# Kernel optimization log

Hardware: AMD Instinct MI355X
Metric: run time of the kernel (lower is better)

The kernel has to match this reference:

```python
import jax, jax.numpy as jnp
import numpy as np

N_NODES = 50000
N_EDGES = 1600000
IN_DIM = 128
N_HEADS = 8
OUT_DIM = 16
LEAKY_SLOPE = 0.2


def setup_inputs() -> dict:
    key = jax.random.key(0)
    k1, k2, k3, k4, k5, k6 = jax.random.split(key, 6)
    x = jax.random.normal(k1, (N_NODES, IN_DIM), dtype=jnp.float32)
    W = jax.random.normal(k2, (N_HEADS * OUT_DIM, IN_DIM), dtype=jnp.float32) * (1.414 / np.sqrt(IN_DIM))
    attn_l = jax.random.normal(k3, (N_HEADS, OUT_DIM), dtype=jnp.float32) * 0.5
    attn_r = jax.random.normal(k4, (N_HEADS, OUT_DIM), dtype=jnp.float32) * 0.5
    src = jax.random.randint(k5, (N_EDGES,), 0, N_NODES, dtype=jnp.int64) if jax.config.jax_enable_x64 else jax.random.randint(k5, (N_EDGES,), 0, N_NODES, dtype=jnp.int32)
    dst = jax.random.randint(k6, (N_EDGES,), 0, N_NODES, dtype=src.dtype)
    return {"x": x, "W": W, "attn_l": attn_l, "attn_r": attn_r, "src": src, "dst": dst}


def reference(x, W, attn_l, attn_r, src, dst):
    n = x.shape[0]
    # fc projection -> [N, H, D]
    ft = (x @ W.T).reshape(n, N_HEADS, OUT_DIM)
    # per-node attention logits (bmm with [H,D,1] vector == contraction over D) -> [N, H]
    a1 = jnp.einsum('nhd,hd->nh', ft, attn_l)
    a2 = jnp.einsum('nhd,hd->nh', ft, attn_r)
    # per-edge score: leaky_relu(a1[src] + a2[dst]) -> [E, H]
    e = jax.nn.leaky_relu(a1[src] + a2[dst], negative_slope=LEAKY_SLOPE)
    # segment softmax over incoming edges of each dst node (numerically stable)
    seg_max = jax.ops.segment_max(e, dst, num_segments=n)          # [N, H]
    seg_max = jnp.where(jnp.isfinite(seg_max), seg_max, 0.0)       # isolated nodes -> 0
    e_exp = jnp.exp(e - seg_max[dst])                              # [E, H]
    denom = jax.ops.segment_sum(e_exp, dst, num_segments=n)        # [N, H]
    alpha = e_exp / denom[dst]                                     # [E, H]
    # weighted scatter-sum of src messages -> [N, H, D]
    msgs = ft[src] * alpha[:, :, None]                             # [E, H, D]
    out = jax.ops.segment_sum(msgs, dst, num_segments=n)
    return out
```

## Files before the change

### kernel.cpp

```cpp
#include <hip/hip_runtime.h>
#include <math.h>

#define N_NODES 50000
#define N_EDGES 1600000
#define IN_DIM 128
#define N_HEADS 8
#define OUT_DIM 16
#define HD 128
#define NBUCK 784
#define BCAP 2560
#define CHUNK 4096
#define BIN_BLOCKS ((N_EDGES + CHUNK - 1) / CHUNK)
#define NTILE 3125
#define PBLK ((NTILE + 3) / 4)
#define TROW 132
#define LOG2E 1.4426950408889634f
#define NPH 7
#define AGG_BLOCKS 1024
#define AGG_WAVES (AGG_BLOCKS * 4)
#define NPW 13

typedef __attribute__((ext_vector_type(8))) short bf16x8;
typedef __attribute__((ext_vector_type(4))) float f32x4;

__device__ __forceinline__ unsigned short f2bf(float f) {
    union { float f; unsigned int u; } v; v.f = f;
    unsigned int u = v.u;
    unsigned int r = (u + 0x7fffu + ((u >> 16) & 1u)) >> 16;
    return (unsigned short)r;
}

__device__ __forceinline__ void scan_nbuck_excl(int* arr, int* part) {
    int t = threadIdx.x;
    int v0 = 0, v1 = 0, v2 = 0, v3 = 0, cs = 0;
    if (t < NBUCK / 4) {
        v0 = arr[4 * t]; v1 = arr[4 * t + 1]; v2 = arr[4 * t + 2]; v3 = arr[4 * t + 3];
        cs = v0 + v1 + v2 + v3;
    }
    part[t] = cs;
    __syncthreads();
    for (int d = 1; d < 256; d <<= 1) {
        int u = (t >= d) ? part[t - d] : 0;
        __syncthreads();
        part[t] += u;
        __syncthreads();
    }
    if (t < NBUCK / 4) {
        int run = part[t] - cs;
        arr[4 * t] = run; run += v0;
        arr[4 * t + 1] = run; run += v1;
        arr[4 * t + 2] = run; run += v2;
        arr[4 * t + 3] = run;
    }
    __syncthreads();
}

__global__ void k_prep(const float* __restrict__ W, unsigned short* __restrict__ Wb,
                       int* __restrict__ bucket_cnt, int* __restrict__ ovf_cnt,
                       unsigned short* __restrict__ ftb, float* __restrict__ a1) {
    int g = blockIdx.x * 256 + threadIdx.x;
    if (g < NBUCK) bucket_cnt[g] = 0;
    if (g == 0) *ovf_cnt = 0;
    if (g < 64) ((unsigned int*)(ftb + (size_t)N_NODES * HD))[g] = 0u;
    if (g >= 64 && g < 64 + N_HEADS)
        a1[(size_t)N_NODES * N_HEADS + (g - 64)] = __int_as_float(0xff800000);
    if (g >= (HD * IN_DIM) / 4) return;
    float4 v = ((const float4*)W)[g];
    ushort4 us;
    us.x = f2bf(v.x); us.y = f2bf(v.y); us.z = f2bf(v.z); us.w = f2bf(v.w);
    ((ushort4*)Wb)[g] = us;
}

__global__ __launch_bounds__(256) void k_proj_bin(
    const float* __restrict__ x, const unsigned short* __restrict__ Wb,
    const float* __restrict__ attn_l, const float* __restrict__ attn_r,
    unsigned short* __restrict__ ftb, float* __restrict__ a1, float* __restrict__ a2,
    const int* __restrict__ src, const int* __restrict__ dst,
    unsigned int* __restrict__ region, int* __restrict__ bucket_cnt,
    int* __restrict__ ovf_cnt, unsigned int* __restrict__ ovf) {
    __shared__ __align__(16) char smem[4 * 16 * TROW * 4];
    int tid = threadIdx.x;

    if (blockIdx.x < PBLK) {
        int wid  = tid >> 6;
        int tile = blockIdx.x * 4 + wid;
        if (tile >= NTILE) return;
        int lane = tid & 63;
        int m = lane & 15, q = lane >> 4;
        int node0 = tile * 16;

        const float* xr = x + (size_t)(node0 + m) * IN_DIM + q * 8;
        float4 xa[4][2];
#pragma unroll
        for (int ks = 0; ks < 4; ks++) {
            xa[ks][0] = *(const float4*)(xr + ks * 32);
            xa[ks][1] = *(const float4*)(xr + ks * 32 + 4);
        }
        bf16x8 afr[4];
#pragma unroll
        for (int ks = 0; ks < 4; ks++) {
            afr[ks][0] = (short)f2bf(xa[ks][0].x); afr[ks][1] = (short)f2bf(xa[ks][0].y);
            afr[ks][2] = (short)f2bf(xa[ks][0].z); afr[ks][3] = (short)f2bf(xa[ks][0].w);
            afr[ks][4] = (short)f2bf(xa[ks][1].x); afr[ks][5] = (short)f2bf(xa[ks][1].y);
            afr[ks][6] = (short)f2bf(xa[ks][1].z); afr[ks][7] = (short)f2bf(xa[ks][1].w);
        }

        float* tl = (float*)smem + wid * (16 * TROW);

#pragma unroll
        for (int h = 0; h < N_HEADS; h++) {
            const unsigned short* wrow = Wb + (size_t)(h * 16 + m) * IN_DIM + q * 8;
            f32x4 c = {0.f, 0.f, 0.f, 0.f};
#pragma unroll
            for (int ks = 0; ks < 4; ks++) {
                bf16x8 bfr = *(const bf16x8*)(wrow + ks * 32);
                c = __builtin_amdgcn_mfma_f32_16x16x32_bf16(afr[ks], bfr, c, 0, 0, 0);
            }
#pragma unroll
            for (int r = 0; r < 4; r++)
                tl[(q * 4 + r) * TROW + h * 16 + m] = c[r];
        }

        int nd = lane & 15;
#pragma unroll
        for (int hi = 0; hi < 2; hi++) {
            int hh = (lane >> 4) + hi * 4;
            const float4* rowv = (const float4*)(tl + nd * TROW + hh * 16);
            const float4* alv  = (const float4*)(attn_l + hh * OUT_DIM);
            const float4* arv  = (const float4*)(attn_r + hh * OUT_DIM);
            float sl = 0.f, sr = 0.f;
#pragma unroll
            for (int d4 = 0; d4 < 4; d4++) {
                float4 fv = rowv[d4];
                float4 al = alv[d4];
                float4 ar = arv[d4];
                sl += fv.x * al.x + fv.y * al.y + fv.z * al.z + fv.w * al.w;
                sr += fv.x * ar.x + fv.y * ar.y + fv.z * ar.z + fv.w * ar.w;
            }
            a1[(node0 + nd) * N_HEADS + hh] = sl * LOG2E;
            a2[(node0 + nd) * N_HEADS + hh] = sr * LOG2E;
        }

#pragma unroll
        for (int p = 0; p < 4; p++) {
            int r = p * 4 + q;
            const float* srcp = tl + r * TROW + m * 8;
            float4 f0 = *(const float4*)(srcp);
            float4 f1 = *(const float4*)(srcp + 4);
            ushort4 u0, u1;
            u0.x = f2bf(f0.x); u0.y = f2bf(f0.y); u0.z = f2bf(f0.z); u0.w = f2bf(f0.w);
            u1.x = f2bf(f1.x); u1.y = f2bf(f1.y); u1.z = f2bf(f1.z); u1.w = f2bf(f1.w);
            ushort4* dstp = (ushort4*)(ftb + (size_t)(node0 + r) * HD + m * 8);
            dstp[0] = u0;
            dstp[1] = u1;
        }
    } else {
        unsigned int* stage = (unsigned int*)smem;
        int* hist  = (int*)(smem + 16384);
        int* delta = (int*)(smem + 19520);
        int* part  = (int*)(smem + 22656);

        int t = tid;
        int base = (blockIdx.x - PBLK) * CHUNK;
        int nvalid = min(CHUNK, N_EDGES - base);

        for (int i = t; i < NBUCK; i += 256) hist[i] = 0;
        __syncthreads();

        unsigned int mypack[CHUNK / 256];
#pragma unroll
        for (int k = 0; k < CHUNK / 256; k++) {
            int i = t + k * 256;
            if (i < nvalid) {
                int s = src[base + i];
                int d = dst[base + i];
                unsigned int p = ((unsigned int)d << 16) | (unsigned int)s;
                mypack[k] = p;
                atomicAdd(&hist[d >> 6], 1);
            }
        }
        __syncthreads();
        for (int i = t; i < NBUCK; i += 256) {
            int h = hist[i];
            delta[i] = (h > 0) ? atomicAdd(&bucket_cnt[i], h) : 0;
        }
        __syncthreads();
        scan_nbuck_excl(hist, part);
        for (int i = t; i < NBUCK; i += 256) delta[i] -= hist[i];
        __syncthreads();
#pragma unroll
        for (int k = 0; k < CHUNK / 256; k++) {
            int i = t + k * 256;
            if (i < nvalid) {
                unsigned int p = mypack[k];
                int slot = atomicAdd(&hist[p >> 22], 1);
                stage[slot] = p;
            }
        }
        __syncthreads();
        for (int i = t; i < nvalid; i += 256) {
            unsigned int p = stage[i];
            int b = p >> 22;
            int pos = delta[b] + i;
            if (pos < BCAP) region[(size_t)b * BCAP + pos] = p;
            else { int o = atomicAdd(ovf_cnt, 1); ovf[o] = p; }
        }
    }
}

__global__ __launch_bounds__(256) void k_place(
    const unsigned int* __restrict__ region, const int* __restrict__ bucket_cnt,
    const int* __restrict__ ovf_cnt, const unsigned int* __restrict__ ovf,
    int* __restrict__ nps, unsigned short* __restrict__ esrc) {
    int b = blockIdx.x;
    int t = threadIdx.x;
    __shared__ int sb[NBUCK], part[256];
    __shared__ int hist[512], sc[512], curs[64 * NPH];
    __shared__ unsigned short sstage[BCAP];

    for (int i = t; i < NBUCK; i += 256) sb[i] = bucket_cnt[i];
    for (int i = t; i < 512; i += 256) hist[i] = 0;
    __syncthreads();
    scan_nbuck_excl(sb, part);

    int truec = bucket_cnt[b];
    int base_b = sb[b];
    int rc = min(truec, BCAP);
    bool fits = (truec <= BCAP);
    const unsigned int* reg = region + (size_t)b * BCAP;

    for (int i = t; i < rc; i += 256) {
        unsigned int p = reg[i];
        int key = (int)((p >> 16) & 63) * NPH + (int)((p & 0xffffu) >> 13);
        atomicAdd(&hist[key], 1);
    }
    int no = 0;
    if (truec > BCAP) {
        no = *ovf_cnt;
        for (int i = t; i < no; i += 256)
            if ((int)(ovf[i] >> 22) == b) {
                unsigned int p = ovf[i];
                int key = (int)((p >> 16) & 63) * NPH + (int)((p & 0xffffu) >> 13);
                atomicAdd(&hist[key], 1);
            }
    }
    __syncthreads();

    {
        int h0 = hist[2 * t], h1 = hist[2 * t + 1];
        int ps = h0 + h1;
        part[t] = ps;
        __syncthreads();
        for (int d = 1; d < 256; d <<= 1) {
            int u = (t >= d) ? part[t - d] : 0;
            __syncthreads();
            part[t] += u;
            __syncthreads();
        }
        int run = part[t] - ps;
        sc[2 * t] = run;
        sc[2 * t + 1] = run + h0;
    }
    __syncthreads();

    for (int i = t; i < 64 * NPH; i += 256) curs[i] = base_b + sc[i];
    for (int i = t; i < 512; i += 256) {
        int nl = i >> 3, p = i & 7;
        int node = b * 64 + nl;
        if (node < N_NODES) {
            int v = (p < NPH) ? sc[nl * NPH + p] : sc[(nl + 1) * NPH];
            nps[node * 8 + p] = base_b + v;
        }
    }
    __syncthreads();

    for (int i = t; i < rc; i += 256) {
        unsigned int p = reg[i];
        int key = (int)((p >> 16) & 63) * NPH + (int)((p & 0xffffu) >> 13);
        int pos = atomicAdd(&curs[key], 1);
        if (fits) sstage[pos - base_b] = (unsigned short)(p & 0xffffu);
        else      esrc[pos] = (unsigned short)(p & 0xffffu);
    }
    if (truec > BCAP) {
        for (int i = t; i < no; i += 256) {
            unsigned int p = ovf[i];
            if ((int)(p >> 22) == b) {
                int key = (int)((p >> 16) & 63) * NPH + (int)((p & 0xffffu) >> 13);
                int pos = atomicAdd(&curs[key], 1);
                esrc[pos] = (unsigned short)(p & 0xffffu);
            }
        }
    }
    __syncthreads();
    if (fits) {
        for (int i = t; i < truec; i += 256)
            esrc[base_b + i] = sstage[i];
    }
}

__global__ __launch_bounds__(256, 4) void k_aggregate(
    const unsigned short* __restrict__ ftb, const float* __restrict__ a1,
    const float* __restrict__ a2, const int* __restrict__ nps,
    const unsigned short* __restrict__ esrc, float* __restrict__ out) {
    int wid  = threadIdx.x >> 6;
    int lane = threadIdx.x & 63;
    int gw = blockIdx.x * 4 + wid;
    int hl = lane >> 3;
    int dimoff = lane * 2;

    int node_l = gw + lane * AGG_WAVES;
    bool vld = (lane < NPW) && (node_l < N_NODES);

    float accx[NPW], accy[NPW], l[NPW], a2h[NPW];
#pragma unroll
    for (int i = 0; i < NPW; i++) {
        accx[i] = 0.f; accy[i] = 0.f; l[i] = 0.f;
        int node = gw + i * AGG_WAVES;
        a2h[i] = (node < N_NODES) ? a2[node * N_HEADS + hl] : 0.f;
    }

    for (int p = 0; p < NPH; p++) {
        int stv = vld ? nps[node_l * 8 + p] : 0;
        int env = vld ? nps[node_l * 8 + p + 1] : 0;
#pragma unroll
        for (int i = 0; i < NPW; i++) {
            int st = __builtin_amdgcn_readlane(stv, i);
            int en = __builtin_amdgcn_readlane(env, i);
            for (int base = st; base < en; base += 64) {
                int nbc = en - base; if (nbc > 64) nbc = 64;
                int v = (int)esrc[base + lane];
                int sv = (lane < nbc) ? v : N_NODES;
                for (int done = 0; done < nbc; done += 8) {
                    float a1v[8]; unsigned int pv[8];
#pragma unroll
                    for (int k = 0; k < 8; k++) {
                        int s = __builtin_amdgcn_readlane(sv, done + k);
                        a1v[k] = a1[(size_t)s * N_HEADS + hl];
                        pv[k]  = *(const unsigned int*)(ftb + (size_t)s * HD + dimoff);
                    }
#pragma unroll
                    for (int k = 0; k < 8; k++) {
                        float tt = a1v[k] + a2h[i];
                        float u = fmaxf(tt, 0.2f * tt);
                        float e;
                        asm("v_exp_f32 %0, %1" : "=v"(e) : "v"(u));
                        l[i] += e;
                        accx[i] = fmaf(e, __uint_as_float(pv[k] << 16), accx[i]);
                        accy[i] = fmaf(e, __uint_as_float(pv[k] & 0xffff0000u), accy[i]);
                    }
                }
            }
        }
    }

    int d0v = vld ? nps[node_l * 8 + 0] : 0;
    int d7v = vld ? nps[node_l * 8 + 7] : 0;
#pragma unroll
    for (int i = 0; i < NPW; i++) {
        int node = gw + i * AGG_WAVES;
        if (node >= N_NODES) break;
        int deg = __builtin_amdgcn_readlane(d7v, i) - __builtin_amdgcn_readlane(d0v, i);
        float invl = (deg > 0) ? 1.f / l[i] : 0.f;
        float2 o; o.x = accx[i] * invl; o.y = accy[i] * invl;
        *(float2*)(out + (size_t)node * HD + dimoff) = o;
    }
}

extern "C" void kernel_launch(void* const* d_in, const int* in_sizes, int n_in,
                              void* d_out, int out_size, void* d_ws, size_t ws_size,
                              hipStream_t stream) {
    const float* x      = (const float*)d_in[0];
    const float* W      = (const float*)d_in[1];
    const float* attn_l = (const float*)d_in[2];
    const float* attn_r = (const float*)d_in[3];
    const int*   src    = (const int*)d_in[4];
    const int*   dst    = (const int*)d_in[5];
    float* out = (float*)d_out;

    char* ws = (char*)d_ws;
    size_t o = 0;
    auto alloc = [&](size_t bytes) -> char* {
        char* p = ws + o;
        o = (o + bytes + 255) & ~(size_t)255;
        return p;
    };
    unsigned short* ftb  = (unsigned short*)alloc((size_t)(N_NODES + 1) * HD * 2);
    float* a1            = (float*)alloc((size_t)(N_NODES + 1) * N_HEADS * 4);
    float* a2            = (float*)alloc((size_t)N_NODES * N_HEADS * 4);
    unsigned short* Wb   = (unsigned short*)alloc((size_t)HD * IN_DIM * 2);
    unsigned int* region = (unsigned int*)alloc((size_t)NBUCK * BCAP * 4);
    int* bucket_cnt      = (int*)alloc((size_t)NBUCK * 4);
    int* ovf_cnt         = (int*)alloc(4);
    unsigned int* ovf    = (unsigned int*)alloc((size_t)N_EDGES * 4);
    int* nps             = (int*)alloc((size_t)N_NODES * 8 * 4);
    unsigned short* esrc = (unsigned short*)alloc((size_t)N_EDGES * 2 + 256);

    (void)in_sizes; (void)n_in; (void)out_size; (void)ws_size;

    k_prep<<<16, 256, 0, stream>>>(W, Wb, bucket_cnt, ovf_cnt, ftb, a1);
    k_proj_bin<<<PBLK + BIN_BLOCKS, 256, 0, stream>>>(
        x, Wb, attn_l, attn_r, ftb, a1, a2,
        src, dst, region, bucket_cnt, ovf_cnt, ovf);
    k_place<<<NBUCK, 256, 0, stream>>>(region, bucket_cnt, ovf_cnt, ovf, nps, esrc);
    k_aggregate<<<AGG_BLOCKS, 256, 0, stream>>>(ftb, a1, a2, nps, esrc, out);
}
```

Baseline: 232.2 us.

## Reorder edge list phase-major globally and stream contiguous node ranges per wave

```diff
diff --git a/kernel.cpp b/kernel.cpp
--- a/kernel.cpp
+++ b/kernel.cpp
@@ -16,6 +16,7 @@
 #define TROW 132
 #define LOG2E 1.4426950408889634f
 #define NPH 7
+#define NB2 (NPH * NBUCK)
 #define AGG_BLOCKS 1024
 #define AGG_WAVES (AGG_BLOCKS * 4)
 #define NPW 13
@@ -55,11 +56,35 @@
     __syncthreads();
 }
 
+__device__ __forceinline__ void scan_flat_excl(int* arr, int n, int* part) {
+    int t = threadIdx.x;
+    int K = (n + 255) / 256;
+    int base = t * K;
+    int cs = 0;
+    for (int k = 0; k < K; k++) { int idx = base + k; if (idx < n) cs += arr[idx]; }
+    part[t] = cs;
+    __syncthreads();
+    for (int d = 1; d < 256; d <<= 1) {
+        int u = (t >= d) ? part[t - d] : 0;
+        __syncthreads();
+        part[t] += u;
+        __syncthreads();
+    }
+    int run = part[t] - cs;
+    for (int k = 0; k < K; k++) {
+        int idx = base + k;
+        if (idx < n) { int v = arr[idx]; arr[idx] = run; run += v; }
+    }
+    __syncthreads();
+}
+
 __global__ void k_prep(const float* __restrict__ W, unsigned short* __restrict__ Wb,
-                       int* __restrict__ bucket_cnt, int* __restrict__ ovf_cnt,
+                       int* __restrict__ bucket_cnt, int* __restrict__ cntp,
+                       int* __restrict__ ovf_cnt,
                        unsigned short* __restrict__ ftb, float* __restrict__ a1) {
     int g = blockIdx.x * 256 + threadIdx.x;
     if (g < NBUCK) bucket_cnt[g] = 0;
+    if (g < NB2) cntp[g] = 0;
     if (g == 0) *ovf_cnt = 0;
     if (g < 64) ((unsigned int*)(ftb + (size_t)N_NODES * HD))[g] = 0u;
     if (g >= 64 && g < 64 + N_HEADS)
@@ -77,7 +102,7 @@
     unsigned short* __restrict__ ftb, float* __restrict__ a1, float* __restrict__ a2,
     const int* __restrict__ src, const int* __restrict__ dst,
     unsigned int* __restrict__ region, int* __restrict__ bucket_cnt,
-    int* __restrict__ ovf_cnt, unsigned int* __restrict__ ovf) {
+    int* __restrict__ cntp, int* __restrict__ ovf_cnt, unsigned int* __restrict__ ovf) {
     __shared__ __align__(16) char smem[4 * 16 * TROW * 4];
     int tid = threadIdx.x;
 
@@ -177,6 +202,7 @@
                 unsigned int p = ((unsigned int)d << 16) | (unsigned int)s;
                 mypack[k] = p;
                 atomicAdd(&hist[d >> 6], 1);
+                atomicAdd(&cntp[(s >> 13) * NBUCK + (d >> 6)], 1);
             }
         }
         __syncthreads();
@@ -210,28 +236,30 @@
 
 __global__ __launch_bounds__(256) void k_place(
     const unsigned int* __restrict__ region, const int* __restrict__ bucket_cnt,
-    const int* __restrict__ ovf_cnt, const unsigned int* __restrict__ ovf,
-    int* __restrict__ nps, unsigned short* __restrict__ esrc) {
+    const int* __restrict__ cntp, const int* __restrict__ ovf_cnt,
+    const unsigned int* __restrict__ ovf,
+    int* __restrict__ nps2, unsigned short* __restrict__ esrc) {
     int b = blockIdx.x;
     int t = threadIdx.x;
-    __shared__ int sb[NBUCK], part[256];
-    __shared__ int hist[512], sc[512], curs[64 * NPH];
+    __shared__ int cpb[NB2], part[256];
+    __shared__ int hist[NPH * 64];
+    __shared__ int curs[NPH * 64];
+    __shared__ int gstart[NPH], lstart[NPH], phtot[NPH];
     __shared__ unsigned short sstage[BCAP];
 
-    for (int i = t; i < NBUCK; i += 256) sb[i] = bucket_cnt[i];
-    for (int i = t; i < 512; i += 256) hist[i] = 0;
-    __syncthreads();
-    scan_nbuck_excl(sb, part);
+    for (int i = t; i < NB2; i += 256) cpb[i] = cntp[i];
+    for (int i = t; i < NPH * 64; i += 256) hist[i] = 0;
+    __syncthreads();
+    scan_flat_excl(cpb, NB2, part);
 
     int truec = bucket_cnt[b];
-    int base_b = sb[b];
     int rc = min(truec, BCAP);
     bool fits = (truec <= BCAP);
     const unsigned int* reg = region + (size_t)b * BCAP;
 
     for (int i = t; i < rc; i += 256) {
-        unsigned int p = reg[i];
-        int key = (int)((p >> 16) & 63) * NPH + (int)((p & 0xffffu) >> 13);
+        unsigned int pk = reg[i];
+        int key = (int)((pk & 0xffffu) >> 13) * 64 + (int)((pk >> 16) & 63);
         atomicAdd(&hist[key], 1);
     }
     int no = 0;
@@ -239,68 +267,105 @@
         no = *ovf_cnt;
         for (int i = t; i < no; i += 256)
             if ((int)(ovf[i] >> 22) == b) {
-                unsigned int p = ovf[i];
-                int key = (int)((p >> 16) & 63) * NPH + (int)((p & 0xffffu) >> 13);
+                unsigned int pk = ovf[i];
+                int key = (int)((pk & 0xffffu) >> 13) * 64 + (int)((pk >> 16) & 63);
                 atomicAdd(&hist[key], 1);
             }
     }
     __syncthreads();
-
-    {
-        int h0 = hist[2 * t], h1 = hist[2 * t + 1];
-        int ps = h0 + h1;
-        part[t] = ps;
-        __syncthreads();
-        for (int d = 1; d < 256; d <<= 1) {
-            int u = (t >= d) ? part[t - d] : 0;
-            __syncthreads();
-            part[t] += u;
-            __syncthreads();
-        }
-        int run = part[t] - ps;
-        sc[2 * t] = run;
-        sc[2 * t + 1] = run + h0;
-    }
-    __syncthreads();
-
-    for (int i = t; i < 64 * NPH; i += 256) curs[i] = base_b + sc[i];
-    for (int i = t; i < 512; i += 256) {
-        int nl = i >> 3, p = i & 7;
+    scan_flat_excl(hist, NPH * 64, part);
+
+    if (t < NPH) {
+        gstart[t] = cpb[t * NBUCK + b];
+        lstart[t] = hist[t * 64];
+        phtot[t]  = ((t == NPH - 1) ? truec : hist[(t + 1) * 64]) - hist[t * 64];
+    }
+    __syncthreads();
+
+    for (int i = t; i < NPH * 64; i += 256) {
+        int p = i >> 6, nl = i & 63;
         int node = b * 64 + nl;
-        if (node < N_NODES) {
-            int v = (p < NPH) ? sc[nl * NPH + p] : sc[(nl + 1) * NPH];
-            nps[node * 8 + p] = base_b + v;
-        }
-    }
+        if (node < N_NODES)
+            nps2[(size_t)p * (N_NODES + 1) + node] = gstart[p] + (hist[i] - lstart[p]);
+        curs[i] = fits ? hist[i] : (gstart[p] + hist[i] - lstart[p]);
+    }
+    if (b == 0 && t < NPH)
+        nps2[(size_t)t * (N_NODES + 1) + N_NODES] =
+            (t == NPH - 1) ? N_EDGES : cpb[(t + 1) * NBUCK];
     __syncthreads();
 
     for (int i = t; i < rc; i += 256) {
-        unsigned int p = reg[i];
-        int key = (int)((p >> 16) & 63) * NPH + (int)((p & 0xffffu) >> 13);
+        unsigned int pk = reg[i];
+        int key = (int)((pk & 0xffffu) >> 13) * 64 + (int)((pk >> 16) & 63);
         int pos = atomicAdd(&curs[key], 1);
-        if (fits) sstage[pos - base_b] = (unsigned short)(p & 0xffffu);
-        else      esrc[pos] = (unsigned short)(p & 0xffffu);
+        if (fits) sstage[pos] = (unsigned short)(pk & 0xffffu);
+        else      esrc[pos]  = (unsigned short)(pk & 0xffffu);
     }
     if (truec > BCAP) {
         for (int i = t; i < no; i += 256) {
-            unsigned int p = ovf[i];
-            if ((int)(p >> 22) == b) {
-                int key = (int)((p >> 16) & 63) * NPH + (int)((p & 0xffffu) >> 13);
+            unsigned int pk = ovf[i];
+            if ((int)(pk >> 22) == b) {
+                int key = (int)((pk & 0xffffu) >> 13) * 64 + (int)((pk >> 16) & 63);
                 int pos = atomicAdd(&curs[key], 1);
-                esrc[pos] = (unsigned short)(p & 0xffffu);
+                esrc[pos] = (unsigned short)(pk & 0xffffu);
             }
         }
     }
     __syncthreads();
     if (fits) {
-        for (int i = t; i < truec; i += 256)
-            esrc[base_b + i] = sstage[i];
-    }
-}
+        for (int p = 0; p < NPH; p++)
+            for (int i = t; i < phtot[p]; i += 256)
+                esrc[gstart[p] + i] = sstage[lstart[p] + i];
+    }
+}
+
+template <int KK>
+__device__ __forceinline__ void issue8(int sv, const float* __restrict__ a1,
+                                       const unsigned short* __restrict__ ftb,
+                                       int hl, int dimoff,
+                                       float* a1v, unsigned int* pv) {
+#pragma unroll
+    for (int j = 0; j < 8; j++) {
+        int s = __builtin_amdgcn_readlane(sv, KK + j);
+        a1v[j] = a1[(size_t)s * N_HEADS + hl];
+        pv[j]  = *(const unsigned int*)(ftb + (size_t)s * HD + dimoff);
+    }
+}
+
+#define FLUSH_ADV()                                                         \
+    {                                                                       \
+        _Pragma("unroll")                                                   \
+        for (int q = 0; q < NPW; q++)                                       \
+            if (q == curi) {                                                \
+                accx[q] += tx; accy[q] += ty; lsum[q] += tl;                \
+                cura2 = (q + 1 < NPW) ? a2h[q + 1] : 0.f;                   \
+            }                                                               \
+        tx = ty = tl = 0.f;                                                 \
+    }
+
+#define CONSUME8(AV, PV, KK)                                                \
+    {                                                                       \
+        _Pragma("unroll")                                                   \
+        for (int j = 0; j < 8; j++) {                                       \
+            int pos = cb + (KK) + j;                                        \
+            while (curi < cnt - 1 && pos >= nb_end) {                       \
+                FLUSH_ADV();                                                \
+                curi++;                                                     \
+                nb_end = __builtin_amdgcn_readlane(bnd, curi + 1);          \
+            }                                                               \
+            float tt = AV[j] + cura2;                                       \
+            float uu = fmaxf(tt, 0.2f * tt);                                \
+            float ee;                                                       \
+            asm("v_exp_f32 %0, %1" : "=v"(ee) : "v"(uu));                   \
+            tl += ee;                                                       \
+            tx = fmaf(ee, __uint_as_float(PV[j] << 16), tx);                \
+            ty = fmaf(ee, __uint_as_float(PV[j] & 0xffff0000u), ty);        \
+        }                                                                   \
+    }
 
 __global__ __launch_bounds__(256, 4) void k_aggregate(
     const unsigned short* __restrict__ ftb, const float* __restrict__ a1,
-    const float* __restrict__ a2, const int* __restrict__ nps,
+    const float* __restrict__ a2, const int* __restrict__ nps2,
     const unsigned short* __restrict__ esrc, float* __restrict__ out) {
     int wid  = threadIdx.x >> 6;
     int lane = threadIdx.x & 63;
@@ -308,61 +373,68 @@
     int hl = lane >> 3;
     int dimoff = lane * 2;
 
-    int node_l = gw + lane * AGG_WAVES;
-    bool vld = (lane < NPW) && (node_l < N_NODES);
-
-    float accx[NPW], accy[NPW], l[NPW], a2h[NPW];
+    int n0 = __builtin_amdgcn_readfirstlane((int)(((long long)gw * N_NODES) / AGG_WAVES));
+    int n1 = __builtin_amdgcn_readfirstlane((int)(((long long)(gw + 1) * N_NODES) / AGG_WAVES));
+    int cnt = n1 - n0;
+
+    float accx[NPW], accy[NPW], lsum[NPW], a2h[NPW];
 #pragma unroll
     for (int i = 0; i < NPW; i++) {
-        accx[i] = 0.f; accy[i] = 0.f; l[i] = 0.f;
-        int node = gw + i * AGG_WAVES;
-        a2h[i] = (node < N_NODES) ? a2[node * N_HEADS + hl] : 0.f;
+        accx[i] = 0.f; accy[i] = 0.f; lsum[i] = 0.f;
+        int node = n0 + i; if (node > N_NODES - 1) node = N_NODES - 1;
+        a2h[i] = a2[(size_t)node * N_HEADS + hl];
     }
 
     for (int p = 0; p < NPH; p++) {
-        int stv = vld ? nps[node_l * 8 + p] : 0;
-        int env = vld ? nps[node_l * 8 + p + 1] : 0;
-#pragma unroll
-        for (int i = 0; i < NPW; i++) {
-            int st = __builtin_amdgcn_readlane(stv, i);
-            int en = __builtin_amdgcn_readlane(env, i);
-            for (int base = st; base < en; base += 64) {
-                int nbc = en - base; if (nbc > 64) nbc = 64;
-                int v = (int)esrc[base + lane];
-                int sv = (lane < nbc) ? v : N_NODES;
-                for (int done = 0; done < nbc; done += 8) {
-                    float a1v[8]; unsigned int pv[8];
-#pragma unroll
-                    for (int k = 0; k < 8; k++) {
-                        int s = __builtin_amdgcn_readlane(sv, done + k);
-                        a1v[k] = a1[(size_t)s * N_HEADS + hl];
-                        pv[k]  = *(const unsigned int*)(ftb + (size_t)s * HD + dimoff);
-                    }
-#pragma unroll
-                    for (int k = 0; k < 8; k++) {
-                        float tt = a1v[k] + a2h[i];
-                        float u = fmaxf(tt, 0.2f * tt);
-                        float e;
-                        asm("v_exp_f32 %0, %1" : "=v"(e) : "v"(u));
-                        l[i] += e;
-                        accx[i] = fmaf(e, __uint_as_float(pv[k] << 16), accx[i]);
-                        accy[i] = fmaf(e, __uint_as_float(pv[k] & 0xffff0000u), accy[i]);
-                    }
-                }
-            }
-        }
-    }
-
-    int d0v = vld ? nps[node_l * 8 + 0] : 0;
-    int d7v = vld ? nps[node_l * 8 + 7] : 0;
+        const int* P = nps2 + (size_t)p * (N_NODES + 1) + n0;
+        int bidx = lane < cnt ? lane : cnt;
+        int bnd = P[bidx];
+        int pbeg = __builtin_amdgcn_readlane(bnd, 0);
+        int pend = __builtin_amdgcn_readlane(bnd, cnt);
+
+        int curi = 0;
+        int nb_end = __builtin_amdgcn_readlane(bnd, 1);
+        float tx = 0.f, ty = 0.f, tl = 0.f;
+        float cura2 = a2h[0];
+
+        for (int cb = pbeg; cb < pend; cb += 64) {
+            int nbc = pend - cb; if (nbc > 64) nbc = 64;
+            int v = (int)esrc[cb + lane];
+            int sv = (lane < nbc) ? v : N_NODES;
+
+            float a1A[8], a1B[8];
+            unsigned int pA[8], pB[8];
+            issue8<0>(sv, a1, ftb, hl, dimoff, a1A, pA);
+            if (nbc > 8)  issue8<8>(sv, a1, ftb, hl, dimoff, a1B, pB);
+            CONSUME8(a1A, pA, 0);
+            if (nbc > 16) issue8<16>(sv, a1, ftb, hl, dimoff, a1A, pA);
+            if (nbc > 8)  CONSUME8(a1B, pB, 8);
+            if (nbc > 24) issue8<24>(sv, a1, ftb, hl, dimoff, a1B, pB);
+            if (nbc > 16) CONSUME8(a1A, pA, 16);
+            if (nbc > 32) issue8<32>(sv, a1, ftb, hl, dimoff, a1A, pA);
+            if (nbc > 24) CONSUME8(a1B, pB, 24);
+            if (nbc > 40) issue8<40>(sv, a1, ftb, hl, dimoff, a1B, pB);
+            if (nbc > 32) CONSUME8(a1A, pA, 32);
+            if (nbc > 48) issue8<48>(sv, a1, ftb, hl, dimoff, a1A, pA);
+            if (nbc > 40) CONSUME8(a1B, pB, 40);
+            if (nbc > 56) issue8<56>(sv, a1, ftb, hl, dimoff, a1B, pB);
+            if (nbc > 48) CONSUME8(a1A, pA, 48);
+            if (nbc > 56) CONSUME8(a1B, pB, 56);
+        }
+        for (;;) {
+            FLUSH_ADV();
+            if (curi >= cnt - 1) break;
+            curi++;
+        }
+    }
+
 #pragma unroll
     for (int i = 0; i < NPW; i++) {
-        int node = gw + i * AGG_WAVES;
-        if (node >= N_NODES) break;
-        int deg = __builtin_amdgcn_readlane(d7v, i) - __builtin_amdgcn_readlane(d0v, i);
-        float invl = (deg > 0) ? 1.f / l[i] : 0.f;
-        float2 o; o.x = accx[i] * invl; o.y = accy[i] * invl;
-        *(float2*)(out + (size_t)node * HD + dimoff) = o;
+        if (i < cnt) {
+            float invl = (lsum[i] > 0.f) ? 1.f / lsum[i] : 0.f;
+            float2 o; o.x = accx[i] * invl; o.y = accy[i] * invl;
+            *(float2*)(out + (size_t)(n0 + i) * HD + dimoff) = o;
+        }
     }
 }
 
@@ -390,17 +462,18 @@
     unsigned short* Wb   = (unsigned short*)alloc((size_t)HD * IN_DIM * 2);
     unsigned int* region = (unsigned int*)alloc((size_t)NBUCK * BCAP * 4);
     int* bucket_cnt      = (int*)alloc((size_t)NBUCK * 4);
+    int* cntp            = (int*)alloc((size_t)NB2 * 4);
     int* ovf_cnt         = (int*)alloc(4);
     unsigned int* ovf    = (unsigned int*)alloc((size_t)N_EDGES * 4);
-    int* nps             = (int*)alloc((size_t)N_NODES * 8 * 4);
+    int* nps2            = (int*)alloc((size_t)NPH * (N_NODES + 1) * 4);
     unsigned short* esrc = (unsigned short*)alloc((size_t)N_EDGES * 2 + 256);
 
     (void)in_sizes; (void)n_in; (void)out_size; (void)ws_size;
 
-    k_prep<<<16, 256, 0, stream>>>(W, Wb, bucket_cnt, ovf_cnt, ftb, a1);
+    k_prep<<<32, 256, 0, stream>>>(W, Wb, bucket_cnt, cntp, ovf_cnt, ftb, a1);
     k_proj_bin<<<PBLK + BIN_BLOCKS, 256, 0, stream>>>(
         x, Wb, attn_l, attn_r, ftb, a1, a2,
-        src, dst, region, bucket_cnt, ovf_cnt, ovf);
-    k_place<<<NBUCK, 256, 0, stream>>>(region, bucket_cnt, ovf_cnt, ovf, nps, esrc);
-    k_aggregate<<<AGG_BLOCKS, 256, 0, stream>>>(ftb, a1, a2, nps, esrc, out);
-}
+        src, dst, region, bucket_cnt, cntp, ovf_cnt, ovf);
+    k_place<<<NBUCK, 256, 0, stream>>>(region, bucket_cnt, cntp, ovf_cnt, ovf, nps2, esrc);
+    k_aggregate<<<AGG_BLOCKS, 256, 0, stream>>>(ftb, a1, a2, nps2, esrc, out);
+}
```

Result: slower. 330.8 us (+42.5%).
